# Kernel optimization log

Hardware: AMD Instinct MI355X
Metric: run time of the kernel (lower is better)

## Reference

```python
import jax, jax.numpy as jnp
import numpy as np
import math

B, Q, K, D = 32, 2048, 2048, 128


def setup_inputs() -> dict:
    key = jax.random.key(0)
    k1, k2, k3, k4 = jax.random.split(key, 4)
    return {
        "queries": jax.random.normal(k1, (B, Q, D), dtype=jnp.float32),
        "keys": jax.random.normal(k2, (B, K, D), dtype=jnp.float32),
        "values": jax.random.normal(k3, (B, K, D), dtype=jnp.float32),
        "valid_len": jax.random.randint(k4, (B,), 0, Q, dtype=jnp.int32),
    }


def reference(queries, keys, values, valid_len):
    d = queries.shape[-1]
    # [B, Q, K] scores
    scores = jnp.einsum("bqd,bkd->bqk", queries, keys) / math.sqrt(d)
    # Faithful to source: mask is over the QUERY dim (X.size(1) of [B,Q,K]);
    # rows with q >= valid_len[b] are set entirely to -1e5 before softmax.
    row_mask = jnp.arange(scores.shape[1]) < valid_len[:, None]  # [B, Q]
    scores = jnp.where(row_mask[:, :, None], scores, -100000.0)
    attn = jax.nn.softmax(scores, axis=-1)  # dropout p=0 -> identity
    return jnp.einsum("bqk,bkv->bqv", attn, values)
```

## Files before the change

### kernel.cpp

```cpp
#include <hip/hip_runtime.h>
#include <stdint.h>

#define NB 32
#define NQ 2048
#define NKK 2048
#define DH 128

constexpr int QBLK = 128;
constexpr int KBLK = 32;
constexpr int NKT2 = NKK / KBLK;
constexpr float C2 = 0.12754299817f;

typedef short short8  __attribute__((ext_vector_type(8)));
typedef float f32x4   __attribute__((ext_vector_type(4)));
typedef float f32x16  __attribute__((ext_vector_type(16)));
typedef uint32_t u32x4 __attribute__((ext_vector_type(4)));

typedef __attribute__((address_space(3))) uint32_t lds_u32_t;
typedef __attribute__((address_space(1))) const uint32_t glb_u32_t;

__device__ __forceinline__ uint16_t f2bf(float x) {
    union { float f; uint32_t u; } v; v.f = x;
    uint32_t r = v.u + 0x7fffu + ((v.u >> 16) & 1u);
    return (uint16_t)(r >> 16);
}

__device__ __forceinline__ void gload16(const void* g, void* l) {
    __builtin_amdgcn_global_load_lds((glb_u32_t*)g, (lds_u32_t*)l, 16, 0, 0);
}

__device__ __forceinline__ uint32_t cvtpk(float lo, float hi) {
    uint32_t d;
    asm("v_cvt_pk_bf16_f32 %0, %1, %2" : "=v"(d) : "v"(lo), "v"(hi));
    return d;
}

__global__ void conv_kf(const float* __restrict__ K, uint16_t* __restrict__ Kf) {
    __shared__ __align__(16) uint16_t T[64][136];
    const int bid = blockIdx.x;
    const int b = bid >> 5, kt = bid & 31;
    const int tid = threadIdx.x;
    const float* src = K + ((size_t)(b * NKK + kt * 64)) * DH;
    #pragma unroll
    for (int r = 0; r < 8; ++r) {
        int flat = r * 256 + tid;
        int row = flat >> 5;
        int c4 = (flat & 31) * 4;
        f32x4 x = *(const f32x4*)(src + (size_t)row * DH + c4);
        T[row][c4 + 0] = f2bf(x[0]);
        T[row][c4 + 1] = f2bf(x[1]);
        T[row][c4 + 2] = f2bf(x[2]);
        T[row][c4 + 3] = f2bf(x[3]);
    }
    __syncthreads();
    uint16_t* dst = Kf + (size_t)bid * 8192;
    #pragma unroll
    for (int r = 0; r < 4; ++r) {
        int c = r * 256 + tid;
        int s = c >> 6, lane = c & 63;
        int ci = s >> 3, t = s & 7;
        int mm = lane & 31, hh = lane >> 5;
        short8 v = *(const short8*)&T[ci * 32 + mm][t * 16 + hh * 8];
        *(short8*)(dst + (size_t)c * 8) = v;
    }
}

__global__ void conv_vf(const float* __restrict__ V, uint16_t* __restrict__ Vf) {
    const int bid = blockIdx.x;
    const int b = bid >> 5, kt = bid & 31;
    const int tid = threadIdx.x;
    const float* src = V + (size_t)b * NKK * DH;
    uint16_t* dst = Vf + (size_t)bid * 8192;
    #pragma unroll
    for (int r = 0; r < 4; ++r) {
        int c = r * 256 + tid;
        int s = c >> 6, lane = c & 63;
        int ci = s >> 3, nt = (s >> 1) & 3, uu = s & 1;
        int m = lane & 31, h = lane >> 5;
        int kb = kt * 64 + ci * 32 + uu * 16 + 4 * h;
        int d = nt * 32 + m;
        short8 w;
        #pragma unroll
        for (int j = 0; j < 8; ++j) {
            int key = kb + (j & 3) + 8 * (j >> 2);
            w[j] = (short)f2bf(src[(size_t)key * DH + d]);
        }
        *(short8*)(dst + (size_t)c * 8) = w;
    }
}

__global__ __launch_bounds__(256, 4)
void attn_fwd(const float* __restrict__ Qg, const uint16_t* __restrict__ Kf,
              const uint16_t* __restrict__ Vf, const int* __restrict__ VL,
              float* __restrict__ Og) {
    __shared__ __align__(16) uint8_t LB[32768];

    const int tid  = threadIdx.x;
    const int wv   = tid >> 6;
    const int lane = tid & 63;
    const int m    = lane & 31;
    const int h    = lane >> 5;

    const int bid = blockIdx.x;
    const int swz = (bid & 7) * 64 + (bid >> 3);
    const int b   = swz >> 4;
    const int qt  = swz & 15;
    const int qb0 = qt * QBLK + wv * 32;

    const int vlen = VL[b];
    const int qrow = qb0 + m;
    const float qsc = (qrow < vlen) ? C2 : 0.0f;

    short8 qf[8];
    {
        const float* qp = Qg + ((size_t)b * NQ + qrow) * DH;
        #pragma unroll
        for (int t = 0; t < 8; ++t) {
            const float* p = qp + t * 16 + h * 8;
            f32x4 x0 = *(const f32x4*)(p);
            f32x4 x1 = *(const f32x4*)(p + 4);
            short8 f;
            f[0] = f2bf(x0[0] * qsc); f[1] = f2bf(x0[1] * qsc);
            f[2] = f2bf(x0[2] * qsc); f[3] = f2bf(x0[3] * qsc);
            f[4] = f2bf(x1[0] * qsc); f[5] = f2bf(x1[1] * qsc);
            f[6] = f2bf(x1[2] * qsc); f[7] = f2bf(x1[3] * qsc);
            qf[t] = f;
        }
    }

    f32x16 oacc[4];
    #pragma unroll
    for (int nt = 0; nt < 4; ++nt)
        #pragma unroll
        for (int r = 0; r < 16; ++r) oacc[nt][r] = 0.0f;
    float lsum = 0.0f;

    const char* kfb = (const char*)Kf + (size_t)b * NKT2 * 8192;
    const char* vfb = (const char*)Vf + (size_t)b * NKT2 * 8192;

    auto stage = [&](int buf, int j) {
        const char* ks = kfb + (size_t)j * 8192;
        const char* vs = vfb + (size_t)j * 8192;
        char* kd = (char*)LB + buf * 16384;
        char* vd = kd + 8192;
        #pragma unroll
        for (int r = 0; r < 2; ++r) {
            gload16(ks + r * 4096 + tid * 16, kd + r * 4096 + tid * 16);
            gload16(vs + r * 4096 + tid * 16, vd + r * 4096 + tid * 16);
        }
    };

    stage(0, 0);
    __syncthreads();

    int cur = 0;
    for (int j = 0; j < NKT2; ++j) {
        if (j + 1 < NKT2) stage(cur ^ 1, j + 1);
        const char* KTc = (const char*)LB + cur * 16384 + (size_t)lane * 16;
        const char* VTc = KTc + 8192;

        f32x16 sacc;
        #pragma unroll
        for (int r = 0; r < 16; ++r) sacc[r] = 0.0f;
        __builtin_amdgcn_s_setprio(1);
        #pragma unroll
        for (int t = 0; t < 8; ++t) {
            short8 kf = *(const short8*)(KTc + t * 1024);
            sacc = __builtin_amdgcn_mfma_f32_32x32x16_bf16(kf, qf[t], sacc, 0, 0, 0);
        }
        __builtin_amdgcn_s_setprio(0);

        short8 pa[2];
        #pragma unroll
        for (int uu = 0; uu < 2; ++uu) {
            float p[8];
            #pragma unroll
            for (int jj = 0; jj < 8; ++jj)
                p[jj] = __builtin_amdgcn_exp2f(sacc[uu * 8 + jj]);
            lsum += ((p[0] + p[1]) + (p[2] + p[3])) + ((p[4] + p[5]) + (p[6] + p[7]));
            union { uint32_t w[4]; short8 s; } pu;
            pu.w[0] = cvtpk(p[0], p[1]);
            pu.w[1] = cvtpk(p[2], p[3]);
            pu.w[2] = cvtpk(p[4], p[5]);
            pu.w[3] = cvtpk(p[6], p[7]);
            pa[uu] = pu.s;
        }

        __builtin_amdgcn_s_setprio(1);
        #pragma unroll
        for (int nt = 0; nt < 4; ++nt) {
            #pragma unroll
            for (int uu = 0; uu < 2; ++uu) {
                short8 vfr = *(const short8*)(VTc + (nt * 2 + uu) * 1024);
                oacc[nt] = __builtin_amdgcn_mfma_f32_32x32x16_bf16(pa[uu], vfr, oacc[nt], 0, 0, 0);
            }
        }
        __builtin_amdgcn_s_setprio(0);

        __syncthreads();
        cur ^= 1;
    }

    float ltot = lsum + __shfl_xor(lsum, 32);
    float* op = Og + ((size_t)b * NQ + qb0) * DH;
    #pragma unroll
    for (int r = 0; r < 16; ++r) {
        const int qr = (r & 3) + 8 * (r >> 2) + 4 * h;
        float lv = __shfl(ltot, qr);
        float inv = 1.0f / lv;
        #pragma unroll
        for (int nt = 0; nt < 4; ++nt)
            op[(size_t)qr * DH + nt * 32 + m] = oacc[nt][r] * inv;
    }
}

extern "C" void kernel_launch(void* const* d_in, const int* in_sizes, int n_in,
                              void* d_out, int out_size, void* d_ws, size_t ws_size,
                              hipStream_t stream) {
    const float* q  = (const float*)d_in[0];
    const float* k  = (const float*)d_in[1];
    const float* v  = (const float*)d_in[2];
    const int*   vl = (const int*)d_in[3];
    float* out = (float*)d_out;

    uint16_t* Kf = (uint16_t*)d_ws;
    uint16_t* Vf = Kf + (size_t)NB * 32 * 8192;

    conv_kf<<<NB * 32, 256, 0, stream>>>(k, Kf);
    conv_vf<<<NB * 32, 256, 0, stream>>>(v, Vf);
    attn_fwd<<<NB * (NQ / QBLK), 256, 0, stream>>>(q, Kf, Vf, vl, out);
}
```

Before: 88.13 us.

## Halve attention block size, merge K/V conversion kernels, move scale into exp

Shrinks the attention work-group from 256 threads (128 query rows) to 128 threads (64 query rows), which doubles the grid and changes the block swizzle and launch bounds. The K and V bf16 conversion kernels are merged into one launch. The query scale and mask factor are now applied inside the exp argument instead of being folded into Q, and the s_setprio hints are removed. The smaller blocks are meant to improve scheduling and cut launch overhead, but each K/V tile is now loaded into LDS for only half as many queries, and each exp gains an extra multiply.

```diff
diff --git a/kernel.cpp b/kernel.cpp
--- a/kernel.cpp
+++ b/kernel.cpp
@@ -6,7 +6,7 @@
 #define NKK 2048
 #define DH 128
 
-constexpr int QBLK = 128;
+constexpr int QBLK = 64;
 constexpr int KBLK = 32;
 constexpr int NKT2 = NKK / KBLK;
 constexpr float C2 = 0.12754299817f;
@@ -35,61 +35,62 @@
     return d;
 }
 
-__global__ void conv_kf(const float* __restrict__ K, uint16_t* __restrict__ Kf) {
+__global__ void conv_kv(const float* __restrict__ K, const float* __restrict__ V,
+                        uint16_t* __restrict__ Kf, uint16_t* __restrict__ Vf) {
     __shared__ __align__(16) uint16_t T[64][136];
-    const int bid = blockIdx.x;
-    const int b = bid >> 5, kt = bid & 31;
+    const int bid0 = blockIdx.x;
     const int tid = threadIdx.x;
-    const float* src = K + ((size_t)(b * NKK + kt * 64)) * DH;
-    #pragma unroll
-    for (int r = 0; r < 8; ++r) {
-        int flat = r * 256 + tid;
-        int row = flat >> 5;
-        int c4 = (flat & 31) * 4;
-        f32x4 x = *(const f32x4*)(src + (size_t)row * DH + c4);
-        T[row][c4 + 0] = f2bf(x[0]);
-        T[row][c4 + 1] = f2bf(x[1]);
-        T[row][c4 + 2] = f2bf(x[2]);
-        T[row][c4 + 3] = f2bf(x[3]);
-    }
-    __syncthreads();
-    uint16_t* dst = Kf + (size_t)bid * 8192;
-    #pragma unroll
-    for (int r = 0; r < 4; ++r) {
-        int c = r * 256 + tid;
-        int s = c >> 6, lane = c & 63;
-        int ci = s >> 3, t = s & 7;
-        int mm = lane & 31, hh = lane >> 5;
-        short8 v = *(const short8*)&T[ci * 32 + mm][t * 16 + hh * 8];
-        *(short8*)(dst + (size_t)c * 8) = v;
-    }
-}
-
-__global__ void conv_vf(const float* __restrict__ V, uint16_t* __restrict__ Vf) {
-    const int bid = blockIdx.x;
-    const int b = bid >> 5, kt = bid & 31;
-    const int tid = threadIdx.x;
-    const float* src = V + (size_t)b * NKK * DH;
-    uint16_t* dst = Vf + (size_t)bid * 8192;
-    #pragma unroll
-    for (int r = 0; r < 4; ++r) {
-        int c = r * 256 + tid;
-        int s = c >> 6, lane = c & 63;
-        int ci = s >> 3, nt = (s >> 1) & 3, uu = s & 1;
-        int m = lane & 31, h = lane >> 5;
-        int kb = kt * 64 + ci * 32 + uu * 16 + 4 * h;
-        int d = nt * 32 + m;
-        short8 w;
-        #pragma unroll
-        for (int j = 0; j < 8; ++j) {
-            int key = kb + (j & 3) + 8 * (j >> 2);
-            w[j] = (short)f2bf(src[(size_t)key * DH + d]);
-        }
-        *(short8*)(dst + (size_t)c * 8) = w;
-    }
-}
-
-__global__ __launch_bounds__(256, 4)
+    if (bid0 < NB * 32) {
+        const int bid = bid0;
+        const int b = bid >> 5, kt = bid & 31;
+        const float* src = K + ((size_t)(b * NKK + kt * 64)) * DH;
+        #pragma unroll
+        for (int r = 0; r < 8; ++r) {
+            int flat = r * 256 + tid;
+            int row = flat >> 5;
+            int c4 = (flat & 31) * 4;
+            f32x4 x = *(const f32x4*)(src + (size_t)row * DH + c4);
+            T[row][c4 + 0] = f2bf(x[0]);
+            T[row][c4 + 1] = f2bf(x[1]);
+            T[row][c4 + 2] = f2bf(x[2]);
+            T[row][c4 + 3] = f2bf(x[3]);
+        }
+        __syncthreads();
+        uint16_t* dst = Kf + (size_t)bid * 8192;
+        #pragma unroll
+        for (int r = 0; r < 4; ++r) {
+            int c = r * 256 + tid;
+            int s = c >> 6, lane = c & 63;
+            int ci = s >> 3, t = s & 7;
+            int mm = lane & 31, hh = lane >> 5;
+            short8 v = *(const short8*)&T[ci * 32 + mm][t * 16 + hh * 8];
+            *(short8*)(dst + (size_t)c * 8) = v;
+        }
+    } else {
+        const int bid = bid0 - NB * 32;
+        const int b = bid >> 5, kt = bid & 31;
+        const float* src = V + (size_t)b * NKK * DH;
+        uint16_t* dst = Vf + (size_t)bid * 8192;
+        #pragma unroll
+        for (int r = 0; r < 4; ++r) {
+            int c = r * 256 + tid;
+            int s = c >> 6, lane = c & 63;
+            int ci = s >> 3, nt = (s >> 1) & 3, uu = s & 1;
+            int m = lane & 31, h = lane >> 5;
+            int kb = kt * 64 + ci * 32 + uu * 16 + 4 * h;
+            int d = nt * 32 + m;
+            short8 w;
+            #pragma unroll
+            for (int j = 0; j < 8; ++j) {
+                int key = kb + (j & 3) + 8 * (j >> 2);
+                w[j] = (short)f2bf(src[(size_t)key * DH + d]);
+            }
+            *(short8*)(dst + (size_t)c * 8) = w;
+        }
+    }
+}
+
+__global__ __launch_bounds__(128, 2)
 void attn_fwd(const float* __restrict__ Qg, const uint16_t* __restrict__ Kf,
               const uint16_t* __restrict__ Vf, const int* __restrict__ VL,
               float* __restrict__ Og) {
@@ -102,28 +103,25 @@
     const int h    = lane >> 5;
 
     const int bid = blockIdx.x;
-    const int swz = (bid & 7) * 64 + (bid >> 3);
-    const int b   = swz >> 4;
-    const int qt  = swz & 15;
+    const int swz = (bid & 7) * 128 + (bid >> 3);
+    const int b   = swz >> 5;
+    const int qt  = swz & 31;
     const int qb0 = qt * QBLK + wv * 32;
 
     const int vlen = VL[b];
-    const int qrow = qb0 + m;
-    const float qsc = (qrow < vlen) ? C2 : 0.0f;
+    const float sc = ((qb0 + m) < vlen) ? C2 : 0.0f;
 
     short8 qf[8];
     {
-        const float* qp = Qg + ((size_t)b * NQ + qrow) * DH;
+        const float* qp = Qg + ((size_t)b * NQ + qb0 + m) * DH;
         #pragma unroll
         for (int t = 0; t < 8; ++t) {
             const float* p = qp + t * 16 + h * 8;
             f32x4 x0 = *(const f32x4*)(p);
             f32x4 x1 = *(const f32x4*)(p + 4);
             short8 f;
-            f[0] = f2bf(x0[0] * qsc); f[1] = f2bf(x0[1] * qsc);
-            f[2] = f2bf(x0[2] * qsc); f[3] = f2bf(x0[3] * qsc);
-            f[4] = f2bf(x1[0] * qsc); f[5] = f2bf(x1[1] * qsc);
-            f[6] = f2bf(x1[2] * qsc); f[7] = f2bf(x1[3] * qsc);
+            f[0] = f2bf(x0[0]); f[1] = f2bf(x0[1]); f[2] = f2bf(x0[2]); f[3] = f2bf(x0[3]);
+            f[4] = f2bf(x1[0]); f[5] = f2bf(x1[1]); f[6] = f2bf(x1[2]); f[7] = f2bf(x1[3]);
             qf[t] = f;
         }
     }
@@ -144,9 +142,9 @@
         char* kd = (char*)LB + buf * 16384;
         char* vd = kd + 8192;
         #pragma unroll
-        for (int r = 0; r < 2; ++r) {
-            gload16(ks + r * 4096 + tid * 16, kd + r * 4096 + tid * 16);
-            gload16(vs + r * 4096 + tid * 16, vd + r * 4096 + tid * 16);
+        for (int r = 0; r < 4; ++r) {
+            gload16(ks + r * 2048 + tid * 16, kd + r * 2048 + tid * 16);
+            gload16(vs + r * 2048 + tid * 16, vd + r * 2048 + tid * 16);
         }
     };
 
@@ -162,13 +160,11 @@
         f32x16 sacc;
         #pragma unroll
         for (int r = 0; r < 16; ++r) sacc[r] = 0.0f;
-        __builtin_amdgcn_s_setprio(1);
         #pragma unroll
         for (int t = 0; t < 8; ++t) {
             short8 kf = *(const short8*)(KTc + t * 1024);
             sacc = __builtin_amdgcn_mfma_f32_32x32x16_bf16(kf, qf[t], sacc, 0, 0, 0);
         }
-        __builtin_amdgcn_s_setprio(0);
 
         short8 pa[2];
         #pragma unroll
@@ -176,7 +172,7 @@
             float p[8];
             #pragma unroll
             for (int jj = 0; jj < 8; ++jj)
-                p[jj] = __builtin_amdgcn_exp2f(sacc[uu * 8 + jj]);
+                p[jj] = __builtin_amdgcn_exp2f(sacc[uu * 8 + jj] * sc);
             lsum += ((p[0] + p[1]) + (p[2] + p[3])) + ((p[4] + p[5]) + (p[6] + p[7]));
             union { uint32_t w[4]; short8 s; } pu;
             pu.w[0] = cvtpk(p[0], p[1]);
@@ -186,7 +182,6 @@
             pa[uu] = pu.s;
         }
 
-        __builtin_amdgcn_s_setprio(1);
         #pragma unroll
         for (int nt = 0; nt < 4; ++nt) {
             #pragma unroll
@@ -195,7 +190,6 @@
                 oacc[nt] = __builtin_amdgcn_mfma_f32_32x32x16_bf16(pa[uu], vfr, oacc[nt], 0, 0, 0);
             }
         }
-        __builtin_amdgcn_s_setprio(0);
 
         __syncthreads();
         cur ^= 1;
@@ -226,7 +220,6 @@
     uint16_t* Kf = (uint16_t*)d_ws;
     uint16_t* Vf = Kf + (size_t)NB * 32 * 8192;
 
-    conv_kf<<<NB * 32, 256, 0, stream>>>(k, Kf);
-    conv_vf<<<NB * 32, 256, 0, stream>>>(v, Vf);
-    attn_fwd<<<NB * (NQ / QBLK), 256, 0, stream>>>(q, Kf, Vf, vl, out);
-}
+    conv_kv<<<2 * NB * 32, 256, 0, stream>>>(k, v, Kf, Vf);
+    attn_fwd<<<NB * (NQ / QBLK), 128, 0, stream>>>(q, Kf, Vf, vl, out);
+}
```

Measured after the change: 98.79 us. +12.1%, slower.
